# Optimization experiments

Measured on AMD Instinct MI355X. Metric: run time of the kernel, lower is better.

The kernel has to match this reference:

```python
import jax, jax.numpy as jnp
import numpy as np

N_NODES = 50000
N_EDGES = 800000
IN_F = 96
HID = 64
N_CLS = 32


def setup_inputs() -> dict:
    key = jax.random.key(0)
    k1, k2, k3, k4 = jax.random.split(key, 4)
    x = jax.random.normal(k1, (N_NODES, IN_F), dtype=jnp.float32)
    edge_index = jax.random.randint(k2, (2, N_EDGES), 0, N_NODES, dtype=jnp.int64)
    # xavier_uniform init for weights, zeros for bias
    lim1 = float(np.sqrt(6.0 / (IN_F + HID)))
    lim2 = float(np.sqrt(6.0 / (HID + N_CLS)))
    W1 = jax.random.uniform(k3, (IN_F, HID), minval=-lim1, maxval=lim1, dtype=jnp.float32)
    W2 = jax.random.uniform(k4, (HID, N_CLS), minval=-lim2, maxval=lim2, dtype=jnp.float32)
    b1 = jnp.zeros((HID,), dtype=jnp.float32)
    b2 = jnp.zeros((N_CLS,), dtype=jnp.float32)
    return {"x": x, "edge_index": edge_index, "W1": W1, "b1": b1, "W2": W2, "b2": b2}


def _ghost_conv(h, src, dst, W, b, num_nodes):
    # gather neighbor feats per edge, per-edge matmul, scatter-add, bias
    msg = h[src] @ W                                   # [E, out]
    agg = jax.ops.segment_sum(msg, dst, num_segments=num_nodes)  # [N, out]
    return agg + b


def reference(x, edge_index, W1, b1, W2, b2):
    src, dst = edge_index[0], edge_index[1]
    n = x.shape[0]
    h = jax.nn.relu(_ghost_conv(x, src, dst, W1, b1, n))
    # F.dropout(training=False) is identity in eval mode
    out = _ghost_conv(h, src, dst, W2, b2, n)
    return jax.nn.log_softmax(out, axis=1)
```

## Files before the change

### kernel.cpp

```cpp
#include <hip/hip_runtime.h>
#include <hip/hip_bf16.h>
#include <hip/hip_fp8.h>

typedef __attribute__((ext_vector_type(8))) short bf16x8;
typedef __attribute__((ext_vector_type(4))) float f32x4;
typedef __attribute__((ext_vector_type(2))) float f32x2;

#define NBLK 512
#define NBINS_PAD 800
#define BCAP 2048
#define W1LD 104
#define HLD 72
#define GSTRIDE 16
#define CHMAX 1600

__device__ inline unsigned short f2bf(float f) {
    unsigned u = __float_as_uint(f);
    return (unsigned short)((u + 0x7fffu + ((u >> 16) & 1u)) >> 16);
}
__device__ inline unsigned pack2(float a, float b) {
    return (unsigned)f2bf(a) | ((unsigned)f2bf(b) << 16);
}
__device__ inline float blo(unsigned u) { return __uint_as_float(u << 16); }
__device__ inline float bhi(unsigned u) { return __uint_as_float(u & 0xffff0000u); }

__device__ inline void acc8(float* a, uint4 v) {
    a[0] += blo(v.x); a[1] += bhi(v.x);
    a[2] += blo(v.y); a[3] += bhi(v.y);
    a[4] += blo(v.z); a[5] += bhi(v.z);
    a[6] += blo(v.w); a[7] += bhi(v.w);
}

__device__ inline void accf8x4(float* a, unsigned u) {
    f32x2 lo = __builtin_amdgcn_cvt_pk_f32_fp8((int)u, false);
    f32x2 hi = __builtin_amdgcn_cvt_pk_f32_fp8((int)u, true);
    a[0] += lo.x; a[1] += lo.y; a[2] += hi.x; a[3] += hi.y;
}
__device__ inline void accf8(float* a, uint4 v) {
    accf8x4(a, v.x); accf8x4(a + 4, v.y); accf8x4(a + 8, v.z); accf8x4(a + 12, v.w);
}

__global__ __launch_bounds__(256) void fused_front(
        const int* __restrict__ ei, int* __restrict__ gcount, int E, int chunk, int nb,
        const float* __restrict__ W1, const float* __restrict__ W2,
        unsigned short* __restrict__ w2t,
        const float* __restrict__ X,
        unsigned char* __restrict__ y1f8, unsigned* __restrict__ pairs, int Mtiles) {
    __shared__ int hist[NBINS_PAD];
    __shared__ int cur[NBINS_PAD];
    __shared__ unsigned epk[CHMAX];
    __shared__ __attribute__((aligned(16))) unsigned short w1l[64 * W1LD];
    int b = blockIdx.x, t = threadIdx.x;
    if (b < NBLK) {
        for (int i = t; i < NBINS_PAD; i += 256) hist[i] = 0;
        __syncthreads();
        int e0 = b * chunk;
        int n = E - e0; if (n > chunk) n = chunk; if (n < 0) n = 0;
        const int* srcp = ei + e0;
        const int* dstp = ei + E + e0;
        for (int i = t; i < n; i += 256) {
            int s = srcp[i], d = dstp[i];
            epk[i] = (unsigned)s | ((unsigned)d << 16);
            atomicAdd(&hist[d >> 6], 1);
        }
        __syncthreads();
        for (int j = t; j < nb; j += 256) {
            int c = hist[j];
            int bs = j << 11;
            if (c) bs += atomicAdd(&gcount[j * GSTRIDE], c);
            cur[j] = bs;
        }
        __syncthreads();
        for (int i = t; i < n; i += 256) {
            unsigned u = epk[i];
            int d = (int)(u >> 16);
            int j = d >> 6;
            int pos = atomicAdd(&cur[j], 1);
            if (pos < ((j + 1) << 11))
                pairs[pos] = (u & 0xffffu) | ((unsigned)(d & 63) << 16);
        }
        return;
    }
    if (b == NBLK) {
        for (int idx = t; idx < 64 * 32; idx += 256) {
            int n2 = idx / 64, k = idx - n2 * 64;
            w2t[idx] = f2bf(W2[k * 32 + n2]);
        }
        return;
    }
    for (int idx = t; idx < 96 * 64; idx += 256) {
        int n2 = idx / 96, k = idx - n2 * 96;
        w1l[n2 * W1LD + k] = f2bf(W1[k * 64 + n2]);
    }
    __syncthreads();
    int wave = (b - NBLK - 1) * 4 + (t >> 6);
    if (wave >= Mtiles) return;
    int lane = t & 63;
    int l15 = lane & 15, quad = lane >> 4;
    const float* arow = X + (long)(wave * 16 + l15) * 96 + quad * 8;
    f32x4 acc[4] = {{0,0,0,0},{0,0,0,0},{0,0,0,0},{0,0,0,0}};
#pragma unroll
    for (int tt = 0; tt < 3; ++tt) {
        float4 p0 = *(const float4*)(arow + tt * 32);
        float4 p1 = *(const float4*)(arow + tt * 32 + 4);
        union { bf16x8 v; unsigned u[4]; } a;
        a.u[0] = pack2(p0.x, p0.y); a.u[1] = pack2(p0.z, p0.w);
        a.u[2] = pack2(p1.x, p1.y); a.u[3] = pack2(p1.z, p1.w);
#pragma unroll
        for (int nt = 0; nt < 4; ++nt) {
            bf16x8 bfr = *(const bf16x8*)(w1l + (nt * 16 + l15) * W1LD + tt * 32 + quad * 8);
            acc[nt] = __builtin_amdgcn_mfma_f32_16x16x32_bf16(a.v, bfr, acc[nt], 0, 0, 0);
        }
    }
    int mbase = wave * 16 + quad * 4;
#pragma unroll
    for (int nt = 0; nt < 4; ++nt) {
        int col = nt * 16 + l15;
        int pk = __builtin_amdgcn_cvt_pk_fp8_f32(acc[nt][0], acc[nt][1], 0, false);
        pk = __builtin_amdgcn_cvt_pk_fp8_f32(acc[nt][2], acc[nt][3], pk, true);
#pragma unroll
        for (int r = 0; r < 4; ++r)
            y1f8[(long)(mbase + r) * 64 + col] = (unsigned char)((pk >> (8 * r)) & 0xff);
    }
}

__global__ __launch_bounds__(512) void bucket_fused(
        const unsigned* __restrict__ pairs, const int* __restrict__ gcount,
        const uint4* __restrict__ y1f8,
        const float* __restrict__ b1, const unsigned short* __restrict__ w2t,
        int2* __restrict__ noderange, int* __restrict__ srcs,
        unsigned short* __restrict__ y2, int N) {
    __shared__ unsigned spk[BCAP];
    __shared__ int lsrc[BCAP];
    __shared__ int cnt64[64], cur64[64], rs[64], re[64];
    __shared__ __attribute__((aligned(16))) unsigned short htile[64 * HLD];
    int b = blockIdx.x, t = threadIdx.x;
    int base = b << 11;
    int cnt = gcount[b * GSTRIDE]; if (cnt > BCAP) cnt = BCAP;
    if (t < 64) cnt64[t] = 0;
    __syncthreads();
    for (int i = t; i < cnt; i += 512) {
        unsigned p = pairs[base + i];
        spk[i] = p;
        atomicAdd(&cnt64[(p >> 16) & 63], 1);
    }
    __syncthreads();
    if (t < 64) {
        int v = cnt64[t], x = v;
#pragma unroll
        for (int o = 1; o < 64; o <<= 1) {
            int y = __shfl_up(x, o);
            if (t >= o) x += y;
        }
        int excl = x - v;
        cur64[t] = excl;
        rs[t] = excl;
        re[t] = excl + v;
        int node = b * 64 + t;
        if (node < N) noderange[node] = make_int2(base + excl, base + excl + v);
    }
    __syncthreads();
    for (int i = t; i < cnt; i += 512) {
        unsigned p = spk[i];
        int pos = atomicAdd(&cur64[(p >> 16) & 63], 1);
        lsrc[pos] = (int)(p & 0xffffu);
    }
    __syncthreads();
    for (int i = t; i < cnt; i += 512) srcs[base + i] = lsrc[i];

    int dl = t >> 3, sub = t & 7, q = sub & 3, half = sub >> 2;
    int s0 = rs[dl] + half, s1 = re[dl];
    float a[16];
#pragma unroll
    for (int i = 0; i < 16; ++i) a[i] = 0.f;
    const uint4* ybase = y1f8 + q;
    int e = s0;
    for (; e + 7 <= s1; e += 8) {
        uint4 u0 = ybase[(long)lsrc[e] * 4];
        uint4 u1 = ybase[(long)lsrc[e + 2] * 4];
        uint4 u2 = ybase[(long)lsrc[e + 4] * 4];
        uint4 u3 = ybase[(long)lsrc[e + 6] * 4];
        accf8(a, u0); accf8(a, u1); accf8(a, u2); accf8(a, u3);
    }
    for (; e < s1; e += 2) accf8(a, ybase[(long)lsrc[e] * 4]);
#pragma unroll
    for (int i = 0; i < 16; ++i) a[i] += __shfl_xor(a[i], 4);
    if (half == 0) {
        const float* bq = b1 + q * 16;
        float v[16];
#pragma unroll
        for (int j = 0; j < 16; ++j) v[j] = fmaxf(a[j] + bq[j], 0.f);
        uint4 o0, o1;
        o0.x = pack2(v[0], v[1]);   o0.y = pack2(v[2], v[3]);
        o0.z = pack2(v[4], v[5]);   o0.w = pack2(v[6], v[7]);
        o1.x = pack2(v[8], v[9]);   o1.y = pack2(v[10], v[11]);
        o1.z = pack2(v[12], v[13]); o1.w = pack2(v[14], v[15]);
        uint4* hp = (uint4*)(htile + dl * HLD + q * 16);
        hp[0] = o0;
        hp[1] = o1;
    }
    __syncthreads();
    int w = t >> 6;
    if (w < 4) {
        int lane = t & 63;
        int l15 = lane & 15, quad = lane >> 4;
        const unsigned short* arow = htile + (w * 16 + l15) * HLD + quad * 8;
        f32x4 acc2[2] = {{0,0,0,0},{0,0,0,0}};
#pragma unroll
        for (int t2 = 0; t2 < 2; ++t2) {
            bf16x8 af = *(const bf16x8*)(arow + t2 * 32);
#pragma unroll
            for (int nt = 0; nt < 2; ++nt) {
                bf16x8 bfr = *(const bf16x8*)(w2t + (long)(nt * 16 + l15) * 64 + t2 * 32 + quad * 8);
                acc2[nt] = __builtin_amdgcn_mfma_f32_16x16x32_bf16(af, bfr, acc2[nt], 0, 0, 0);
            }
        }
        int mbase = b * 64 + w * 16 + quad * 4;
#pragma unroll
        for (int nt = 0; nt < 2; ++nt) {
            int col = nt * 16 + l15;
#pragma unroll
            for (int r = 0; r < 4; ++r) {
                int n = mbase + r;
                if (n < N) y2[(long)n * 32 + col] = f2bf(acc2[nt][r]);
            }
        }
    }
}

__global__ void gather_lsm(const uint4* __restrict__ y2, const int2* __restrict__ rng,
                           const int* __restrict__ srcs, const float* __restrict__ bias,
                           float* __restrict__ out, int N) {
    int gid = blockIdx.x * blockDim.x + threadIdx.x;
    int n = gid >> 3;
    if (n >= N) return;
    int sub = gid & 7, q = sub & 3, half = sub >> 2;
    int2 r01 = rng[n];
    int s0 = r01.x + half, s1 = r01.y;
    float a[8];
#pragma unroll
    for (int i = 0; i < 8; ++i) a[i] = 0.f;
    const uint4* base = y2 + q;
    int e = s0;
    for (; e + 7 <= s1; e += 8) {
        uint4 u0 = base[(long)srcs[e] * 4];
        uint4 u1 = base[(long)srcs[e + 2] * 4];
        uint4 u2 = base[(long)srcs[e + 4] * 4];
        uint4 u3 = base[(long)srcs[e + 6] * 4];
        acc8(a, u0); acc8(a, u1); acc8(a, u2); acc8(a, u3);
    }
    for (; e < s1; e += 2) acc8(a, base[(long)srcs[e] * 4]);
#pragma unroll
    for (int i = 0; i < 8; ++i) a[i] += __shfl_xor(a[i], 4);
    const float* bq = bias + q * 8;
    float m = -1e30f;
#pragma unroll
    for (int i = 0; i < 8; ++i) { a[i] += bq[i]; m = fmaxf(m, a[i]); }
    m = fmaxf(m, __shfl_xor(m, 1));
    m = fmaxf(m, __shfl_xor(m, 2));
    float s = 0.f;
#pragma unroll
    for (int i = 0; i < 8; ++i) s += __expf(a[i] - m);
    s += __shfl_xor(s, 1);
    s += __shfl_xor(s, 2);
    float ls = m + __logf(s);
    if (half == 0) {
        float* op = out + (long)n * 32 + q * 8;
        float4 o0 = make_float4(a[0] - ls, a[1] - ls, a[2] - ls, a[3] - ls);
        float4 o1 = make_float4(a[4] - ls, a[5] - ls, a[6] - ls, a[7] - ls);
        *(float4*)op = o0;
        *((float4*)op + 1) = o1;
    }
}

extern "C" void kernel_launch(void* const* d_in, const int* in_sizes, int n_in,
                              void* d_out, int out_size, void* d_ws, size_t ws_size,
                              hipStream_t stream) {
    const float* x  = (const float*)d_in[0];
    const int*   ei = (const int*)d_in[1];
    const float* W1 = (const float*)d_in[2];
    const float* b1 = (const float*)d_in[3];
    const float* W2 = (const float*)d_in[4];
    const float* b2 = (const float*)d_in[5];
    float* out = (float*)d_out;

    const int N = in_sizes[0] / 96;
    const int E = in_sizes[1] / 2;
    const int nb = (N + 63) / 64;
    const int chunk = (E + NBLK - 1) / NBLK;

    char* p = (char*)d_ws;
    unsigned char*  y1f8 = (unsigned char*)p;     p += (size_t)N * 64;
    unsigned short* y2   = (unsigned short*)p;    p += (size_t)N * 32 * 2;
    unsigned short* w2t  = (unsigned short*)p;    p += 64 * 32 * 2;
    int2* noderange = (int2*)p;                   p += (size_t)N * 8;
    int* gcount = (int*)p;                        p += (size_t)nb * GSTRIDE * 4;
    unsigned* pairs = (unsigned*)p;               p += (size_t)nb * BCAP * 4;
    int* srcs   = (int*)p;                        p += (size_t)nb * BCAP * 4;

    const int Mtiles = N / 16;
    const int gblocks = (Mtiles + 3) / 4;

    hipMemsetAsync(gcount, 0, (size_t)nb * GSTRIDE * 4, stream);
    fused_front<<<NBLK + 1 + gblocks, 256, 0, stream>>>(
        ei, gcount, E, chunk, nb, W1, W2, w2t, x, y1f8, pairs, Mtiles);
    bucket_fused<<<nb, 512, 0, stream>>>(pairs, gcount, (const uint4*)y1f8,
                                         b1, w2t, noderange, srcs, y2, N);
    gather_lsm<<<(N * 8 + 255) / 256, 256, 0, stream>>>(
        (const uint4*)y2, noderange, srcs, b2, out, N);
}
```

Baseline: 149.1 us.

## Precompute bf16 weight transposes in a prep kernel, replacing memset and per-block LDS staging

```diff
diff --git a/kernel.cpp b/kernel.cpp
--- a/kernel.cpp
+++ b/kernel.cpp
@@ -9,7 +9,6 @@
 #define NBLK 512
 #define NBINS_PAD 800
 #define BCAP 2048
-#define W1LD 104
 #define HLD 72
 #define GSTRIDE 16
 #define CHMAX 1600
@@ -40,16 +39,31 @@
     accf8x4(a, v.x); accf8x4(a + 4, v.y); accf8x4(a + 8, v.z); accf8x4(a + 12, v.w);
 }
 
+__global__ __launch_bounds__(256) void prep(
+        const float* __restrict__ W1, const float* __restrict__ W2,
+        unsigned short* __restrict__ w1t, unsigned short* __restrict__ w2t,
+        int* __restrict__ gcount, int ng) {
+    int gid = blockIdx.x * 256 + threadIdx.x;
+    int stride = gridDim.x * 256;
+    for (int i = gid; i < ng; i += stride) gcount[i] = 0;
+    for (int i = gid; i < 64 * 96; i += stride) {
+        int n = i / 96, k = i - n * 96;
+        w1t[i] = f2bf(W1[k * 64 + n]);
+    }
+    for (int i = gid; i < 64 * 32; i += stride) {
+        int n = i / 64, k = i - n * 64;
+        w2t[i] = f2bf(W2[k * 32 + n]);
+    }
+}
+
 __global__ __launch_bounds__(256) void fused_front(
         const int* __restrict__ ei, int* __restrict__ gcount, int E, int chunk, int nb,
-        const float* __restrict__ W1, const float* __restrict__ W2,
-        unsigned short* __restrict__ w2t,
+        const uint4* __restrict__ w1t4,
         const float* __restrict__ X,
         unsigned char* __restrict__ y1f8, unsigned* __restrict__ pairs, int Mtiles) {
     __shared__ int hist[NBINS_PAD];
     __shared__ int cur[NBINS_PAD];
     __shared__ unsigned epk[CHMAX];
-    __shared__ __attribute__((aligned(16))) unsigned short w1l[64 * W1LD];
     int b = blockIdx.x, t = threadIdx.x;
     if (b < NBLK) {
         for (int i = t; i < NBINS_PAD; i += 256) hist[i] = 0;
@@ -81,19 +95,7 @@
         }
         return;
     }
-    if (b == NBLK) {
-        for (int idx = t; idx < 64 * 32; idx += 256) {
-            int n2 = idx / 64, k = idx - n2 * 64;
-            w2t[idx] = f2bf(W2[k * 32 + n2]);
-        }
-        return;
-    }
-    for (int idx = t; idx < 96 * 64; idx += 256) {
-        int n2 = idx / 96, k = idx - n2 * 96;
-        w1l[n2 * W1LD + k] = f2bf(W1[k * 64 + n2]);
-    }
-    __syncthreads();
-    int wave = (b - NBLK - 1) * 4 + (t >> 6);
+    int wave = (b - NBLK) * 4 + (t >> 6);
     if (wave >= Mtiles) return;
     int lane = t & 63;
     int l15 = lane & 15, quad = lane >> 4;
@@ -108,8 +110,9 @@
         a.u[2] = pack2(p1.x, p1.y); a.u[3] = pack2(p1.z, p1.w);
 #pragma unroll
         for (int nt = 0; nt < 4; ++nt) {
-            bf16x8 bfr = *(const bf16x8*)(w1l + (nt * 16 + l15) * W1LD + tt * 32 + quad * 8);
-            acc[nt] = __builtin_amdgcn_mfma_f32_16x16x32_bf16(a.v, bfr, acc[nt], 0, 0, 0);
+            union { uint4 u; bf16x8 v; } wb;
+            wb.u = w1t4[(nt * 16 + l15) * 12 + tt * 4 + quad];
+            acc[nt] = __builtin_amdgcn_mfma_f32_16x16x32_bf16(a.v, wb.v, acc[nt], 0, 0, 0);
         }
     }
     int mbase = wave * 16 + quad * 4;
@@ -292,6 +295,7 @@
     char* p = (char*)d_ws;
     unsigned char*  y1f8 = (unsigned char*)p;     p += (size_t)N * 64;
     unsigned short* y2   = (unsigned short*)p;    p += (size_t)N * 32 * 2;
+    unsigned short* w1t  = (unsigned short*)p;    p += 64 * 96 * 2;
     unsigned short* w2t  = (unsigned short*)p;    p += 64 * 32 * 2;
     int2* noderange = (int2*)p;                   p += (size_t)N * 8;
     int* gcount = (int*)p;                        p += (size_t)nb * GSTRIDE * 4;
@@ -301,9 +305,9 @@
     const int Mtiles = N / 16;
     const int gblocks = (Mtiles + 3) / 4;
 
-    hipMemsetAsync(gcount, 0, (size_t)nb * GSTRIDE * 4, stream);
-    fused_front<<<NBLK + 1 + gblocks, 256, 0, stream>>>(
-        ei, gcount, E, chunk, nb, W1, W2, w2t, x, y1f8, pairs, Mtiles);
+    prep<<<32, 256, 0, stream>>>(W1, W2, w1t, w2t, gcount, nb * GSTRIDE);
+    fused_front<<<NBLK + gblocks, 256, 0, stream>>>(
+        ei, gcount, E, chunk, nb, (const uint4*)w1t, x, y1f8, pairs, Mtiles);
     bucket_fused<<<nb, 512, 0, stream>>>(pairs, gcount, (const uint4*)y1f8,
                                          b1, w2t, noderange, srcs, y2, N);
     gather_lsm<<<(N * 8 + 255) / 256, 256, 0, stream>>>(
```

Result: faster. 141.3 us (-5.3%).
